# Kernel optimization log

Measured on AMD Instinct MI355X. Metric: run time of the kernel, lower is better.

## Reference

```python
import jax, jax.numpy as jnp
from jax import lax
import numpy as np

B, C, H, W = 16, 128, 128, 128
S1 = C // 2   # 64, LKA3 branch channels
S2 = C - S1   # 64, LKA5 branch channels
EPS = 1e-6
DN = ('NCHW', 'OIHW', 'NCHW')


def _dw(x, w, b, pad, dil=1):
    # depthwise conv; torch weight layout (C,1,kh,kw) == OIHW with groups=C
    y = lax.conv_general_dilated(x, w, (1, 1), [(pad[0], pad[0]), (pad[1], pad[1])],
                                 rhs_dilation=(dil, dil), dimension_numbers=DN,
                                 feature_group_count=w.shape[0])
    return y + b[None, :, None, None]


def _pw(x, w, b):
    # 1x1 pointwise conv
    y = lax.conv_general_dilated(x, w, (1, 1), [(0, 0), (0, 0)], dimension_numbers=DN)
    return y + b[None, :, None, None]


def setup_inputs() -> dict:
    key = jax.random.key(0)
    ks = iter(jax.random.split(key, 40))
    rn = lambda shape, s=0.05: jax.random.normal(next(ks), shape, jnp.float32) * s
    inp = {
        'x': jax.random.normal(next(ks), (B, C, H, W), jnp.float32),
        'ln_w': jnp.ones((C,), jnp.float32),
        'ln_b': jnp.zeros((C,), jnp.float32),
        'scale': rn((1, C, 1, 1)),
        'pf_w': rn((2 * C, C, 1, 1)), 'pf_b': rn((2 * C,)),
        # LKA3: dw(1x3) -> dw(3x1) -> dw5 dil2 -> 1x1
        'lka3_w1': rn((S1, 1, 1, 3)), 'lka3_b1': rn((S1,)),
        'lka3_w2': rn((S1, 1, 3, 1)), 'lka3_b2': rn((S1,)),
        'lka3_w3': rn((S1, 1, 5, 5)), 'lka3_b3': rn((S1,)),
        'lka3_w4': rn((S1, S1, 1, 1)), 'lka3_b4': rn((S1,)),
        # LKA5: dw5 -> dw7 dil2 -> 1x1
        'lka5_w1': rn((S2, 1, 5, 5)), 'lka5_b1': rn((S2,)),
        'lka5_w2': rn((S2, 1, 7, 7)), 'lka5_b2': rn((S2,)),
        'lka5_w3': rn((S2, S2, 1, 1)), 'lka5_b3': rn((S2,)),
        # gating convs
        'x3a_w': rn((S1, 1, 1, 3)), 'x3a_b': rn((S1,)),
        'x3b_w': rn((S1, 1, 3, 1)), 'x3b_b': rn((S1,)),
        'x5_w': rn((S2, 1, 5, 5)), 'x5_b': rn((S2,)),
        'pl_w': rn((C, C, 1, 1)), 'pl_b': rn((C,)),
    }
    return inp


def reference(x, ln_w, ln_b, scale, pf_w, pf_b,
              lka3_w1, lka3_b1, lka3_w2, lka3_b2, lka3_w3, lka3_b3, lka3_w4, lka3_b4,
              lka5_w1, lka5_b1, lka5_w2, lka5_b2, lka5_w3, lka5_b3,
              x3a_w, x3a_b, x3b_w, x3b_b, x5_w, x5_b, pl_w, pl_b):
    shortcut = x
    # channels_first LayerNorm (biased variance over channel dim)
    u = jnp.mean(x, axis=1, keepdims=True)
    s = jnp.mean((x - u) ** 2, axis=1, keepdims=True)
    xn = (x - u) * lax.rsqrt(s + EPS)
    xn = ln_w[None, :, None, None] * xn + ln_b[None, :, None, None]
    # proj_first: C -> 2C
    h = _pw(xn, pf_w, pf_b)
    a, xh = h[:, :C], h[:, C:]
    a1, a2 = a[:, :S1], a[:, S1:]
    # gating branch for a1: 1x3 then 3x1 depthwise
    x3_out = _dw(_dw(a1, x3a_w, x3a_b, (0, 1)), x3b_w, x3b_b, (1, 0))
    # LKA3: dw(1x3)->dw(3x1)->dw5(dil2,pad4)->1x1
    l3 = _dw(a1, lka3_w1, lka3_b1, (0, 1))
    l3 = _dw(l3, lka3_w2, lka3_b2, (1, 0))
    l3 = _dw(l3, lka3_w3, lka3_b3, (4, 4), dil=2)
    l3 = _pw(l3, lka3_w4, lka3_b4)
    attn_1 = l3 * x3_out
    # LKA5: dw5(pad2)->dw7(dil2,pad6)->1x1
    l5 = _dw(a2, lka5_w1, lka5_b1, (2, 2))
    l5 = _dw(l5, lka5_w2, lka5_b2, (6, 6), dil=2)
    l5 = _pw(l5, lka5_w3, lka5_b3)
    attn_2 = l5 * _dw(a2, x5_w, x5_b, (2, 2))
    a = jnp.concatenate([attn_1, attn_2], axis=1)
    out = _pw(xh * a, pl_w, pl_b) * scale + shortcut
    return out
```

## Files before the change

kernel.cpp:

```cpp
#include <hip/hip_runtime.h>
#include <hip/hip_bf16.h>

typedef __hip_bfloat16 bf16;
typedef unsigned short ushort_t;
typedef float f32x4 __attribute__((ext_vector_type(4)));
typedef short bf16x8 __attribute__((ext_vector_type(8)));

#define MFMA16(a, b, c) __builtin_amdgcn_mfma_f32_16x16x32_bf16(a, b, c, 0, 0, 0)

__device__ inline ushort_t f2b(float f) {
  bf16 h = __float2bfloat16(f);
  return __builtin_bit_cast(ushort_t, h);
}
__device__ inline float b2f(ushort_t u) {
  bf16 h = __builtin_bit_cast(bf16, u);
  return __bfloat162float(h);
}
__device__ inline float blo(unsigned d) { return __builtin_bit_cast(float, d << 16); }
__device__ inline float bhi(unsigned d) { return __builtin_bit_cast(float, d & 0xffff0000u); }


__global__ __launch_bounds__(256) void prepack_pf(
    const float* __restrict__ pf_w, ushort_t* __restrict__ pf_wp)
{
  int idx = blockIdx.x * 256 + threadIdx.x;
  int j = idx & 7, lane = (idx >> 3) & 63, kc = (idx >> 9) & 3, t = idx >> 11;
  int oc = t * 16 + (lane & 15), ic = kc * 32 + (lane >> 4) * 8 + j;
  pf_wp[idx] = f2b(pf_w[oc * 128 + ic]);
}

__global__ __launch_bounds__(256) void prepack_small(
    const float* __restrict__ w4, const float* __restrict__ w5,
    const float* __restrict__ plw, ushort_t* __restrict__ dst)
{
  int idx = blockIdx.x * 256 + threadIdx.x;
  if (idx < 8192) {
    const float* src = (idx < 4096) ? w4 : w5;
    int k = idx & 4095;
    int j = k & 7, lane = (k >> 3) & 63, kc = (k >> 9) & 1, t = k >> 10;
    int oc = t * 16 + (lane & 15), ic = kc * 32 + (lane >> 4) * 8 + j;
    dst[idx] = f2b(src[oc * 64 + ic]);
  } else {
    int k = idx - 8192;
    int j = k & 7, lane = (k >> 3) & 63, kc = (k >> 9) & 3, t = k >> 11;
    int oc = t * 16 + (lane & 15), ic = kc * 32 + (lane >> 4) * 8 + j;
    dst[idx] = f2b(plw[oc * 128 + ic]);
  }
}

__global__ __launch_bounds__(256) void ln_pf_mfma(
    const float* __restrict__ x, const float* __restrict__ ln_w,
    const float* __restrict__ ln_b, const ushort_t* __restrict__ pf_wp,
    const float* __restrict__ pf_b, ushort_t* __restrict__ h)
{
  __shared__ __attribute__((aligned(16))) unsigned char sm[34816];
  ushort_t* xs = (ushort_t*)sm;
  float* red = (float*)(sm + 17408);
  float* mrs = (float*)(sm + 17408 + 2048);

  const int tid = threadIdx.x;
  const int p = tid & 63, cg = tid >> 6;
  const int g0 = blockIdx.x * 64;
  const int b = g0 >> 14, hw0 = g0 & 16383;
  const float* xp = x + (long)b * (128L * 16384) + hw0 + p;

  float v[32];
  #pragma unroll
  for (int i = 0; i < 32; ++i) v[i] = xp[(long)(cg * 32 + i) * 16384];
  float s = 0.f, ss = 0.f;
  #pragma unroll
  for (int i = 0; i < 32; ++i) { s += v[i]; ss += v[i] * v[i]; }
  red[cg * 64 + p] = s;
  red[256 + cg * 64 + p] = ss;
  __syncthreads();
  if (tid < 64) {
    float st = red[tid] + red[64 + tid] + red[128 + tid] + red[192 + tid];
    float sst = red[256 + tid] + red[320 + tid] + red[384 + tid] + red[448 + tid];
    float m = st * 0.0078125f;
    float var = sst * 0.0078125f - m * m;
    mrs[tid] = m;
    mrs[64 + tid] = rsqrtf(var + 1e-6f);
  }
  __syncthreads();
  {
    float m = mrs[p], rs = mrs[64 + p];
    #pragma unroll
    for (int i = 0; i < 32; ++i) {
      int c = cg * 32 + i;
      xs[p * 136 + c] = f2b((v[i] - m) * rs * ln_w[c] + ln_b[c]);
    }
  }
  __syncthreads();

  const int l = tid & 63, lm = l & 15, q = l >> 4;
  const int wv = __builtin_amdgcn_readfirstlane(tid >> 6);
  f32x4 acc[4][4];
  #pragma unroll
  for (int a = 0; a < 4; ++a)
    #pragma unroll
    for (int n = 0; n < 4; ++n) acc[a][n] = {0.f, 0.f, 0.f, 0.f};

  #pragma unroll
  for (int kc = 0; kc < 4; ++kc) {
    bf16x8 af[4], bfr[4];
    #pragma unroll
    for (int mt = 0; mt < 4; ++mt)
      af[mt] = *(const bf16x8*)&xs[(mt * 16 + lm) * 136 + kc * 32 + q * 8];
    #pragma unroll
    for (int nt = 0; nt < 4; ++nt)
      bfr[nt] = *(const bf16x8*)&pf_wp[(((wv * 4 + nt) * 4 + kc) * 64 + l) * 8];
    #pragma unroll
    for (int mt = 0; mt < 4; ++mt)
      #pragma unroll
      for (int nt = 0; nt < 4; ++nt)
        acc[mt][nt] = MFMA16(af[mt], bfr[nt], acc[mt][nt]);
  }
  __syncthreads();

  ushort_t* hst = (ushort_t*)sm;
  #pragma unroll
  for (int nt = 0; nt < 4; ++nt) {
    int oc = wv * 64 + nt * 16 + lm;
    float bias = pf_b[oc];
    #pragma unroll
    for (int mt = 0; mt < 4; ++mt) {
      int px0 = mt * 16 + q * 4;
      union { ushort_t u[4]; uint2 w; } pk;
      #pragma unroll
      for (int r = 0; r < 4; ++r) pk.u[r] = f2b(acc[mt][nt][r] + bias);
      *(uint2*)&hst[oc * 68 + px0] = pk.w;
    }
  }
  __syncthreads();
  {
    int px = (tid & 31) * 2;
    int ocb = tid >> 5;
    ushort_t* hp = h + (long)b * 256 * 16384 + hw0 + px;
    #pragma unroll
    for (int i = 0; i < 32; ++i) {
      int oc = ocb + 8 * i;
      *(unsigned*)(hp + (long)oc * 16384) = *(unsigned*)&hst[oc * 68 + px];
    }
  }
}

__global__ __launch_bounds__(256) void dw_branch1_kernel(
    const bf16* __restrict__ hbuf,
    const float* __restrict__ w1, const float* __restrict__ b1,
    const float* __restrict__ w2, const float* __restrict__ b2,
    const float* __restrict__ w3, const float* __restrict__ b3,
    const float* __restrict__ wa, const float* __restrict__ ba,
    const float* __restrict__ wb, const float* __restrict__ bb,
    bf16* __restrict__ d3, bf16* __restrict__ x3o)
{
  __shared__ float sa[18 * 138];
  __shared__ float st1[18 * 136];
  __shared__ float st2[16 * 136];
  __shared__ float su1[10 * 128];

  const int t = blockIdx.x;
  const int band = t & 15, c = (t >> 4) & 63, b = t >> 10;
  const int y0 = band * 8;
  const int tid = threadIdx.x;
  const int col = tid & 127, rhalf = tid >> 7;
  const bf16* ap = hbuf + ((long)b * 256 + c) * 16384;

  float W1[3], W2[3], WA[3], WB[3], W3[25];
  #pragma unroll
  for (int k = 0; k < 3; ++k) {
    W1[k] = w1[c * 3 + k]; W2[k] = w2[c * 3 + k];
    WA[k] = wa[c * 3 + k]; WB[k] = wb[c * 3 + k];
  }
  #pragma unroll
  for (int k = 0; k < 25; ++k) W3[k] = w3[c * 25 + k];
  const float B1 = b1[c], B2 = b2[c], B3 = b3[c], BA = ba[c], BB = bb[c];

  for (int i = tid; i < 18 * 5; i += 256) {
    int r = i / 5, qq = i % 5;
    sa[r * 138 + qq] = 0.f;
    sa[r * 138 + 133 + qq] = 0.f;
  }
  #pragma unroll
  for (int rr = rhalf; rr < 18; rr += 2) {
    int gy = y0 - 5 + rr;
    float v = 0.f;
    if ((unsigned)gy < 128u) v = __bfloat162float(ap[gy * 128 + col]);
    sa[rr * 138 + 5 + col] = v;
  }
  __syncthreads();

  #pragma unroll
  for (int rr = rhalf; rr < 18; rr += 2) {
    int gy = y0 - 5 + rr;
    bool rowok = (unsigned)gy < 128u;
    const float* sr = &sa[rr * 138];
    {
      int xq = col - 4;
      float v = W1[0] * sr[col] + W1[1] * sr[col + 1] + W1[2] * sr[col + 2] + B1;
      st1[rr * 136 + col] = (rowok && (unsigned)xq < 128u) ? v : 0.f;
    }
    if (col < 8) {
      int cc = col + 128, xq = cc - 4;
      float v = W1[0] * sr[cc] + W1[1] * sr[cc + 1] + W1[2] * sr[cc + 2] + B1;
      st1[rr * 136 + cc] = (rowok && (unsigned)xq < 128u) ? v : 0.f;
    }
  }
  #pragma unroll
  for (int r = rhalf; r < 10; r += 2) {
    int gy = y0 - 1 + r;
    const float* sr = &sa[(r + 4) * 138];
    float v = WA[0] * sr[col + 4] + WA[1] * sr[col + 5] + WA[2] * sr[col + 6] + BA;
    su1[r * 128 + col] = ((unsigned)gy < 128u) ? v : 0.f;
  }
  __syncthreads();

  #pragma unroll
  for (int r = rhalf; r < 16; r += 2) {
    int gy = y0 - 4 + r;
    bool rowok = (unsigned)gy < 128u;
    {
      int xq = col - 4;
      float v = W2[0] * st1[r * 136 + col] + W2[1] * st1[(r + 1) * 136 + col] +
                W2[2] * st1[(r + 2) * 136 + col] + B2;
      st2[r * 136 + col] = (rowok && (unsigned)xq < 128u) ? v : 0.f;
    }
    if (col < 8) {
      int cc = col + 128, xq = cc - 4;
      float v = W2[0] * st1[r * 136 + cc] + W2[1] * st1[(r + 1) * 136 + cc] +
                W2[2] * st1[(r + 2) * 136 + cc] + B2;
      st2[r * 136 + cc] = (rowok && (unsigned)xq < 128u) ? v : 0.f;
    }
  }
  __syncthreads();

  bf16* d3p = d3 + ((long)b * 64 + c) * 16384;
  bf16* x3p = x3o + ((long)b * 64 + c) * 16384;
  #pragma unroll
  for (int ro = rhalf; ro < 8; ro += 2) {
    float acc = B3;
    #pragma unroll
    for (int u = 0; u < 5; ++u)
      #pragma unroll
      for (int v = 0; v < 5; ++v)
        acc += W3[u * 5 + v] * st2[(ro + 2 * u) * 136 + col + 2 * v];
    d3p[(y0 + ro) * 128 + col] = __float2bfloat16(acc);

    float xo = WB[0] * su1[ro * 128 + col] + WB[1] * su1[(ro + 1) * 128 + col] +
               WB[2] * su1[(ro + 2) * 128 + col] + BB;
    x3p[(y0 + ro) * 128 + col] = __float2bfloat16(xo);
  }
}

__global__ __launch_bounds__(256) void dw_branch2_kernel(
    const bf16* __restrict__ hbuf,
    const float* __restrict__ w1, const float* __restrict__ b1,
    const float* __restrict__ w2, const float* __restrict__ b2,
    const float* __restrict__ w5, const float* __restrict__ b5,
    bf16* __restrict__ d5, bf16* __restrict__ x5o)
{
  __shared__ ushort_t sa[32 * 160];
  __shared__ float sv[28 * 148];

  const int t = blockIdx.x;
  const int band = t & 7, c = (t >> 3) & 63, b = t >> 9;
  const int y0 = band * 16;
  const int tid = threadIdx.x;
  const bf16* ap = hbuf + ((long)b * 256 + 64 + c) * 16384;

  unsigned* sad = (unsigned*)sa;
  for (int i = tid; i < 32 * 16; i += 256) {
    int r = i >> 4, j = i & 15;
    int dw = (j < 4) ? j : (64 + j);
    sad[r * 80 + dw] = 0u;
  }
  {
    const int lane = tid & 63, w = tid >> 6;
    #pragma unroll
    for (int i = 0; i < 8; ++i) {
      int rr = w + 4 * i;
      int gy = y0 - 8 + rr;
      unsigned val = 0u;
      if ((unsigned)gy < 128u) val = *(const unsigned*)(ap + gy * 128 + lane * 2);
      sad[rr * 80 + 4 + lane] = val;
    }
  }
  __syncthreads();

  {
    float W[25];
    #pragma unroll
    for (int k = 0; k < 25; ++k) W[k] = w1[c * 25 + k];
    const float B1v = b1[c];
    for (int task = tid; task < 28 * 18; task += 256) {
      int r = task / 18, g = task - r * 18;
      int c0 = g * 8;
      float acc[8];
      #pragma unroll
      for (int j = 0; j < 8; ++j) acc[j] = B1v;
      #pragma unroll
      for (int u = 0; u < 5; ++u) {
        const unsigned* sr = sad + (r + u) * 80 + (c0 >> 1);
        unsigned e0 = sr[0], e1 = sr[1], e2 = sr[2], e3 = sr[3], e4 = sr[4], e5 = sr[5];
        float vw[12];
        vw[0] = blo(e0); vw[1] = bhi(e0); vw[2] = blo(e1); vw[3] = bhi(e1);
        vw[4] = blo(e2); vw[5] = bhi(e2); vw[6] = blo(e3); vw[7] = bhi(e3);
        vw[8] = blo(e4); vw[9] = bhi(e4); vw[10] = blo(e5); vw[11] = bhi(e5);
        #pragma unroll
        for (int v5 = 0; v5 < 5; ++v5)
          #pragma unroll
          for (int j = 0; j < 8; ++j)
            acc[j] += W[u * 5 + v5] * vw[j + v5];
      }
      int gy = y0 - 6 + r;
      bool rok = (unsigned)gy < 128u;
      float* svr = &sv[r * 148 + c0];
      #pragma unroll
      for (int j = 0; j < 8; ++j) {
        int xx = c0 + j - 6;
        svr[j] = (rok && (unsigned)xx < 128u) ? acc[j] : 0.f;
      }
    }
  }

  const int tx = tid & 15, ty = tid >> 4;
  const int x0 = tx * 8;
  const int y = y0 + ty;

  {
    float W[25];
    #pragma unroll
    for (int k = 0; k < 25; ++k) W[k] = w5[c * 25 + k];
    float acc[8];
    #pragma unroll
    for (int j = 0; j < 8; ++j) acc[j] = b5[c];
    #pragma unroll
    for (int u = 0; u < 5; ++u) {
      const unsigned* sr = sad + (ty + 6 + u) * 80 + (x0 >> 1);
      unsigned e0 = sr[3], e1 = sr[4], e2 = sr[5], e3 = sr[6], e4 = sr[7], e5 = sr[8];
      float vw[12];
      vw[0] = blo(e0); vw[1] = bhi(e0); vw[2] = blo(e1); vw[3] = bhi(e1);
      vw[4] = blo(e2); vw[5] = bhi(e2); vw[6] = blo(e3); vw[7] = bhi(e3);
      vw[8] = blo(e4); vw[9] = bhi(e4); vw[10] = blo(e5); vw[11] = bhi(e5);
      #pragma unroll
      for (int v5 = 0; v5 < 5; ++v5)
        #pragma unroll
        for (int j = 0; j < 8; ++j)
          acc[j] += W[u * 5 + v5] * vw[j + v5];
    }
    union { ushort_t u[8]; uint4 v; } pk;
    #pragma unroll
    for (int j = 0; j < 8; ++j) pk.u[j] = f2b(acc[j]);
    bf16* x5p = x5o + ((long)b * 64 + c) * 16384;
    *(uint4*)(x5p + y * 128 + x0) = pk.v;
  }
  __syncthreads();

  {
    float W[49];
    #pragma unroll
    for (int k = 0; k < 49; ++k) W[k] = w2[c * 49 + k];
    float acc[8];
    #pragma unroll
    for (int j = 0; j < 8; ++j) acc[j] = b2[c];
    #pragma unroll
    for (int u = 0; u < 7; ++u) {
      const float* svr = &sv[(ty + 2 * u) * 148 + x0];
      float vw[20];
      #pragma unroll
      for (int k = 0; k < 20; ++k) vw[k] = svr[k];
      #pragma unroll
      for (int vv = 0; vv < 7; ++vv)
        #pragma unroll
        for (int j = 0; j < 8; ++j)
          acc[j] += W[u * 7 + vv] * vw[j + 2 * vv];
    }
    union { ushort_t u[8]; uint4 v; } pk;
    #pragma unroll
    for (int j = 0; j < 8; ++j) pk.u[j] = f2b(acc[j]);
    bf16* d5p = d5 + ((long)b * 64 + c) * 16384;
    *(uint4*)(d5p + y * 128 + x0) = pk.v;
  }
}

__global__ __launch_bounds__(256) void final_mfma(
    const ushort_t* __restrict__ h, const ushort_t* __restrict__ d3,
    const ushort_t* __restrict__ x3o, const ushort_t* __restrict__ d5,
    const ushort_t* __restrict__ x5o,
    const ushort_t* __restrict__ w4p, const float* __restrict__ b4,
    const ushort_t* __restrict__ w5p, const float* __restrict__ b5,
    const ushort_t* __restrict__ plwp, const float* __restrict__ plb,
    const float* __restrict__ scale, const float* __restrict__ x,
    float* __restrict__ out)
{
  __shared__ __attribute__((aligned(16))) unsigned char sm[35840];
  ushort_t* A3 = (ushort_t*)sm;
  ushort_t* A5 = (ushort_t*)(sm + 9216);
  ushort_t* gA = (ushort_t*)(sm + 18432);

  const int tid = threadIdx.x;
  const int g0 = blockIdx.x * 64;
  const int b = g0 >> 14, hw0 = g0 & 16383;
  const long base64 = (long)b * 64 * 16384 + hw0;
  const long base256 = (long)b * 256 * 16384 + hw0;
  const int p = tid & 63;

  #pragma unroll
  for (int i = 0; i < 16; ++i) {
    int ch = (tid >> 6) + 4 * i;
    A3[p * 72 + ch] = d3[base64 + (long)ch * 16384 + p];
    A5[p * 72 + ch] = d5[base64 + (long)ch * 16384 + p];
  }
  __syncthreads();

  const int l = tid & 63, lm = l & 15, q = l >> 4;
  const int wv = __builtin_amdgcn_readfirstlane(tid >> 6);

  f32x4 ac1[4], ac2[4];
  #pragma unroll
  for (int n = 0; n < 4; ++n) { ac1[n] = {0.f,0.f,0.f,0.f}; ac2[n] = {0.f,0.f,0.f,0.f}; }
  #pragma unroll
  for (int kc = 0; kc < 2; ++kc) {
    bf16x8 a3f = *(const bf16x8*)&A3[(wv * 16 + lm) * 72 + kc * 32 + q * 8];
    bf16x8 a5f = *(const bf16x8*)&A5[(wv * 16 + lm) * 72 + kc * 32 + q * 8];
    #pragma unroll
    for (int nt = 0; nt < 4; ++nt) {
      bf16x8 bw4 = *(const bf16x8*)&w4p[((nt * 2 + kc) * 64 + l) * 8];
      bf16x8 bw5 = *(const bf16x8*)&w5p[((nt * 2 + kc) * 64 + l) * 8];
      ac1[nt] = MFMA16(a3f, bw4, ac1[nt]);
      ac2[nt] = MFMA16(a5f, bw5, ac2[nt]);
    }
  }

  #pragma unroll
  for (int nt = 0; nt < 4; ++nt) {
    int oc = nt * 16 + lm;
    float bb1 = b4[oc], bb2 = b5[oc];
    #pragma unroll
    for (int r = 0; r < 4; ++r) {
      int px = wv * 16 + q * 4 + r;
      float at1 = (ac1[nt][r] + bb1) * b2f(x3o[base64 + (long)oc * 16384 + px]);
      float at2 = (ac2[nt][r] + bb2) * b2f(x5o[base64 + (long)oc * 16384 + px]);
      float g1 = b2f(h[base256 + (long)(128 + oc) * 16384 + px]) * at1;
      float g2 = b2f(h[base256 + (long)(192 + oc) * 16384 + px]) * at2;
      gA[px * 136 + oc]      = f2b(g1);
      gA[px * 136 + 64 + oc] = f2b(g2);
    }
  }
  __syncthreads();

  f32x4 ap[4][2];
  #pragma unroll
  for (int mt = 0; mt < 4; ++mt) { ap[mt][0] = {0.f,0.f,0.f,0.f}; ap[mt][1] = {0.f,0.f,0.f,0.f}; }
  #pragma unroll
  for (int kc = 0; kc < 4; ++kc) {
    bf16x8 af[4];
    #pragma unroll
    for (int mt = 0; mt < 4; ++mt)
      af[mt] = *(const bf16x8*)&gA[(mt * 16 + lm) * 136 + kc * 32 + q * 8];
    #pragma unroll
    for (int j = 0; j < 2; ++j) {
      bf16x8 bp = *(const bf16x8*)&plwp[(((wv * 2 + j) * 4 + kc) * 64 + l) * 8];
      #pragma unroll
      for (int mt = 0; mt < 4; ++mt)
        ap[mt][j] = MFMA16(af[mt], bp, ap[mt][j]);
    }
  }
  __syncthreads();

  float* outL = (float*)sm;
  #pragma unroll
  for (int j = 0; j < 2; ++j) {
    int oc = (wv * 2 + j) * 16 + lm;
    float sc = scale[oc], bb = plb[oc];
    #pragma unroll
    for (int mt = 0; mt < 4; ++mt) {
      int px0 = mt * 16 + q * 4;
      f32x4 vv;
      #pragma unroll
      for (int r = 0; r < 4; ++r) vv[r] = (ap[mt][j][r] + bb) * sc;
      *(f32x4*)&outL[oc * 68 + px0] = vv;
    }
  }
  __syncthreads();
  {
    const float* xp = x + (long)b * 128 * 16384 + hw0 + p;
    float* op = out + (long)b * 128 * 16384 + hw0 + p;
    #pragma unroll
    for (int i = 0; i < 32; ++i) {
      int oc = (tid >> 6) + 4 * i;
      op[(long)oc * 16384] = outL[oc * 68 + p] + xp[(long)oc * 16384];
    }
  }
}

extern "C" void kernel_launch(void* const* d_in, const int* in_sizes, int n_in,
                              void* d_out, int out_size, void* d_ws, size_t ws_size,
                              hipStream_t stream)
{
  (void)in_sizes; (void)n_in; (void)out_size; (void)ws_size;
  const float* x       = (const float*)d_in[0];
  const float* ln_w    = (const float*)d_in[1];
  const float* ln_b    = (const float*)d_in[2];
  const float* scale   = (const float*)d_in[3];
  const float* pf_w    = (const float*)d_in[4];
  const float* pf_b    = (const float*)d_in[5];
  const float* lka3_w1 = (const float*)d_in[6];
  const float* lka3_b1 = (const float*)d_in[7];
  const float* lka3_w2 = (const float*)d_in[8];
  const float* lka3_b2 = (const float*)d_in[9];
  const float* lka3_w3 = (const float*)d_in[10];
  const float* lka3_b3 = (const float*)d_in[11];
  const float* lka3_w4 = (const float*)d_in[12];
  const float* lka3_b4 = (const float*)d_in[13];
  const float* lka5_w1 = (const float*)d_in[14];
  const float* lka5_b1 = (const float*)d_in[15];
  const float* lka5_w2 = (const float*)d_in[16];
  const float* lka5_b2 = (const float*)d_in[17];
  const float* lka5_w3 = (const float*)d_in[18];
  const float* lka5_b3 = (const float*)d_in[19];
  const float* x3a_w   = (const float*)d_in[20];
  const float* x3a_b   = (const float*)d_in[21];
  const float* x3b_w   = (const float*)d_in[22];
  const float* x3b_b   = (const float*)d_in[23];
  const float* x5_w    = (const float*)d_in[24];
  const float* x5_b    = (const float*)d_in[25];
  const float* pl_w    = (const float*)d_in[26];
  const float* pl_b    = (const float*)d_in[27];
  float* out = (float*)d_out;

  bf16* h   = (bf16*)d_ws;
  bf16* d3  = h + 67108864L;
  bf16* x3o = d3 + 16777216L;
  bf16* d5  = x3o + 16777216L;
  bf16* x5o = d5 + 16777216L;
  ushort_t* pf_wp = (ushort_t*)d_out;
  ushort_t* wsmall = (ushort_t*)d_ws;

  dim3 blk(256);

  prepack_pf<<<128, blk, 0, stream>>>(pf_w, pf_wp);
  ln_pf_mfma<<<4096, blk, 0, stream>>>(x, ln_w, ln_b, pf_wp, pf_b, (ushort_t*)h);

  dw_branch1_kernel<<<16384, blk, 0, stream>>>(
      h, lka3_w1, lka3_b1, lka3_w2, lka3_b2, lka3_w3, lka3_b3,
      x3a_w, x3a_b, x3b_w, x3b_b, d3, x3o);

  dw_branch2_kernel<<<8192, blk, 0, stream>>>(
      h, lka5_w1, lka5_b1, lka5_w2, lka5_b2, x5_w, x5_b, d5, x5o);

  prepack_small<<<96, blk, 0, stream>>>(lka3_w4, lka5_w3, pl_w, wsmall);

  final_mfma<<<4096, blk, 0, stream>>>(
      (const ushort_t*)h, (const ushort_t*)d3, (const ushort_t*)x3o,
      (const ushort_t*)d5, (const ushort_t*)x5o,
      wsmall, lka3_b4, wsmall + 4096, lka5_b3,
      wsmall + 8192, pl_b, scale, x, out);
}
```

Baseline: 589.7 us.

## Restructure LKA3 depthwise branch kernel with 16-row bands and 8-pixel register tiles

Rewrites the first depthwise branch kernel so each block handles a 16-row band instead of 8. This halves the grid and cuts redundant halo reloads. The input tile is kept as packed bf16 in shared memory, and each thread computes 8 horizontal outputs from registers with 16-byte vector stores. Shared memory is aliased between stages to fit, and the gating path now reads straight from the input tile. In exchange, register use and the shared footprint per block go up, which may lower occupancy.

New measurement: 537.0 us. -8.9%, faster.

```diff
diff --git a/kernel.cpp b/kernel.cpp
--- a/kernel.cpp
+++ b/kernel.cpp
@@ -153,101 +153,143 @@
     const float* __restrict__ wb, const float* __restrict__ bb,
     bf16* __restrict__ d3, bf16* __restrict__ x3o)
 {
-  __shared__ float sa[18 * 138];
-  __shared__ float st1[18 * 136];
-  __shared__ float st2[16 * 136];
-  __shared__ float su1[10 * 128];
+  __shared__ __attribute__((aligned(16))) unsigned char smem[28000];
+  float* st1 = (float*)smem;
+  float* st2 = (float*)(smem + 14560);
+  ushort_t* sa = (ushort_t*)(smem + 14560);
+  unsigned* sad = (unsigned*)sa;
 
   const int t = blockIdx.x;
-  const int band = t & 15, c = (t >> 4) & 63, b = t >> 10;
-  const int y0 = band * 8;
+  const int band = t & 7, c = (t >> 3) & 63, b = t >> 9;
+  const int y0 = band * 16;
   const int tid = threadIdx.x;
-  const int col = tid & 127, rhalf = tid >> 7;
   const bf16* ap = hbuf + ((long)b * 256 + c) * 16384;
 
-  float W1[3], W2[3], WA[3], WB[3], W3[25];
-  #pragma unroll
-  for (int k = 0; k < 3; ++k) {
-    W1[k] = w1[c * 3 + k]; W2[k] = w2[c * 3 + k];
-    WA[k] = wa[c * 3 + k]; WB[k] = wb[c * 3 + k];
-  }
-  #pragma unroll
-  for (int k = 0; k < 25; ++k) W3[k] = w3[c * 25 + k];
-  const float B1 = b1[c], B2 = b2[c], B3 = b3[c], BA = ba[c], BB = bb[c];
-
-  for (int i = tid; i < 18 * 5; i += 256) {
-    int r = i / 5, qq = i % 5;
-    sa[r * 138 + qq] = 0.f;
-    sa[r * 138 + 133 + qq] = 0.f;
-  }
-  #pragma unroll
-  for (int rr = rhalf; rr < 18; rr += 2) {
-    int gy = y0 - 5 + rr;
-    float v = 0.f;
-    if ((unsigned)gy < 128u) v = __bfloat162float(ap[gy * 128 + col]);
-    sa[rr * 138 + 5 + col] = v;
-  }
-  __syncthreads();
-
-  #pragma unroll
-  for (int rr = rhalf; rr < 18; rr += 2) {
-    int gy = y0 - 5 + rr;
-    bool rowok = (unsigned)gy < 128u;
-    const float* sr = &sa[rr * 138];
-    {
-      int xq = col - 4;
-      float v = W1[0] * sr[col] + W1[1] * sr[col + 1] + W1[2] * sr[col + 2] + B1;
-      st1[rr * 136 + col] = (rowok && (unsigned)xq < 128u) ? v : 0.f;
-    }
-    if (col < 8) {
-      int cc = col + 128, xq = cc - 4;
-      float v = W1[0] * sr[cc] + W1[1] * sr[cc + 1] + W1[2] * sr[cc + 2] + B1;
-      st1[rr * 136 + cc] = (rowok && (unsigned)xq < 128u) ? v : 0.f;
-    }
-  }
-  #pragma unroll
-  for (int r = rhalf; r < 10; r += 2) {
-    int gy = y0 - 1 + r;
-    const float* sr = &sa[(r + 4) * 138];
-    float v = WA[0] * sr[col + 4] + WA[1] * sr[col + 5] + WA[2] * sr[col + 6] + BA;
-    su1[r * 128 + col] = ((unsigned)gy < 128u) ? v : 0.f;
-  }
-  __syncthreads();
-
-  #pragma unroll
-  for (int r = rhalf; r < 16; r += 2) {
-    int gy = y0 - 4 + r;
-    bool rowok = (unsigned)gy < 128u;
-    {
-      int xq = col - 4;
-      float v = W2[0] * st1[r * 136 + col] + W2[1] * st1[(r + 1) * 136 + col] +
-                W2[2] * st1[(r + 2) * 136 + col] + B2;
-      st2[r * 136 + col] = (rowok && (unsigned)xq < 128u) ? v : 0.f;
-    }
-    if (col < 8) {
-      int cc = col + 128, xq = cc - 4;
-      float v = W2[0] * st1[r * 136 + cc] + W2[1] * st1[(r + 1) * 136 + cc] +
-                W2[2] * st1[(r + 2) * 136 + cc] + B2;
-      st2[r * 136 + cc] = (rowok && (unsigned)xq < 128u) ? v : 0.f;
-    }
-  }
-  __syncthreads();
-
-  bf16* d3p = d3 + ((long)b * 64 + c) * 16384;
-  bf16* x3p = x3o + ((long)b * 64 + c) * 16384;
-  #pragma unroll
-  for (int ro = rhalf; ro < 8; ro += 2) {
-    float acc = B3;
-    #pragma unroll
-    for (int u = 0; u < 5; ++u)
-      #pragma unroll
-      for (int v = 0; v < 5; ++v)
-        acc += W3[u * 5 + v] * st2[(ro + 2 * u) * 136 + col + 2 * v];
-    d3p[(y0 + ro) * 128 + col] = __float2bfloat16(acc);
-
-    float xo = WB[0] * su1[ro * 128 + col] + WB[1] * su1[(ro + 1) * 128 + col] +
-               WB[2] * su1[(ro + 2) * 128 + col] + BB;
-    x3p[(y0 + ro) * 128 + col] = __float2bfloat16(xo);
+  for (int i = tid; i < 26 * 16; i += 256) {
+    int r = i >> 4, j = i & 15;
+    int dw = (j < 4) ? j : (64 + j);
+    sad[r * 80 + dw] = 0u;
+  }
+  {
+    const int lane = tid & 63, w = tid >> 6;
+    #pragma unroll
+    for (int i = 0; i < 7; ++i) {
+      int rr = w + 4 * i;
+      if (rr < 26) {
+        int gy = y0 - 5 + rr;
+        unsigned val = 0u;
+        if ((unsigned)gy < 128u) val = *(const unsigned*)(ap + gy * 128 + lane * 2);
+        sad[rr * 80 + 4 + lane] = val;
+      }
+    }
+  }
+  __syncthreads();
+
+  {
+    float W0 = w1[c * 3], Wm = w1[c * 3 + 1], Wp = w1[c * 3 + 2];
+    const float B1v = b1[c];
+    for (int task = tid; task < 26 * 17; task += 256) {
+      int r = task / 17, g = task - r * 17;
+      int c0 = g * 8;
+      const unsigned* sr = sad + r * 80 + (c0 >> 1) + 1;
+      unsigned e0 = sr[0], e1 = sr[1], e2 = sr[2], e3 = sr[3], e4 = sr[4], e5 = sr[5];
+      float vw[12];
+      vw[0] = blo(e0); vw[1] = bhi(e0); vw[2] = blo(e1); vw[3] = bhi(e1);
+      vw[4] = blo(e2); vw[5] = bhi(e2); vw[6] = blo(e3); vw[7] = bhi(e3);
+      vw[8] = blo(e4); vw[9] = bhi(e4); vw[10] = blo(e5); vw[11] = bhi(e5);
+      int gy = y0 - 5 + r;
+      bool rok = (unsigned)gy < 128u;
+      float* dst = &st1[r * 140 + c0];
+      #pragma unroll
+      for (int j = 0; j < 8; ++j) {
+        float v = W0 * vw[j + 1] + Wm * vw[j + 2] + Wp * vw[j + 3] + B1v;
+        int xx = c0 - 4 + j;
+        dst[j] = (rok && (unsigned)xx < 128u) ? v : 0.f;
+      }
+    }
+  }
+
+  const int tx = tid & 15, ty = tid >> 4;
+  const int x0 = tx * 8;
+  const int y = y0 + ty;
+
+  {
+    float A0 = wa[c * 3], A1 = wa[c * 3 + 1], A2 = wa[c * 3 + 2];
+    float Bv0 = wb[c * 3], Bv1 = wb[c * 3 + 1], Bv2 = wb[c * 3 + 2];
+    const float BAv = ba[c], BBv = bb[c];
+    float su[3][8];
+    #pragma unroll
+    for (int dy = 0; dy < 3; ++dy) {
+      int gy2 = y - 1 + dy;
+      int srow = ty + 4 + dy;
+      const unsigned* sr = sad + srow * 80 + (x0 >> 1) + 3;
+      unsigned e0 = sr[0], e1 = sr[1], e2 = sr[2], e3 = sr[3], e4 = sr[4], e5 = sr[5];
+      float vw[12];
+      vw[0] = blo(e0); vw[1] = bhi(e0); vw[2] = blo(e1); vw[3] = bhi(e1);
+      vw[4] = blo(e2); vw[5] = bhi(e2); vw[6] = blo(e3); vw[7] = bhi(e3);
+      vw[8] = blo(e4); vw[9] = bhi(e4); vw[10] = blo(e5); vw[11] = bhi(e5);
+      bool rok = (unsigned)gy2 < 128u;
+      #pragma unroll
+      for (int j = 0; j < 8; ++j) {
+        float v = A0 * vw[j + 1] + A1 * vw[j + 2] + A2 * vw[j + 3] + BAv;
+        su[dy][j] = rok ? v : 0.f;
+      }
+    }
+    union { ushort_t u[8]; uint4 v; } pk;
+    #pragma unroll
+    for (int j = 0; j < 8; ++j)
+      pk.u[j] = f2b(Bv0 * su[0][j] + Bv1 * su[1][j] + Bv2 * su[2][j] + BBv);
+    bf16* x3p = x3o + ((long)b * 64 + c) * 16384;
+    *(uint4*)(x3p + y * 128 + x0) = pk.v;
+  }
+  __syncthreads();
+
+  {
+    float W0 = w2[c * 3], Wm = w2[c * 3 + 1], Wp = w2[c * 3 + 2];
+    const float B2v = b2[c];
+    for (int task = tid; task < 24 * 17; task += 256) {
+      int q = task / 17, g = task - q * 17;
+      int c0 = g * 8;
+      const float* r0 = &st1[q * 140 + c0];
+      const float* r1 = &st1[(q + 1) * 140 + c0];
+      const float* r2 = &st1[(q + 2) * 140 + c0];
+      int gy = y0 - 4 + q;
+      bool rok = (unsigned)gy < 128u;
+      float* dst = &st2[q * 140 + c0];
+      #pragma unroll
+      for (int j = 0; j < 8; ++j) {
+        float v = W0 * r0[j] + Wm * r1[j] + Wp * r2[j] + B2v;
+        int xx = c0 - 4 + j;
+        dst[j] = (rok && (unsigned)xx < 128u) ? v : 0.f;
+      }
+    }
+  }
+  __syncthreads();
+
+  {
+    float W[25];
+    #pragma unroll
+    for (int k = 0; k < 25; ++k) W[k] = w3[c * 25 + k];
+    float acc[8];
+    #pragma unroll
+    for (int j = 0; j < 8; ++j) acc[j] = b3[c];
+    #pragma unroll
+    for (int u = 0; u < 5; ++u) {
+      const float* svr = &st2[(ty + 2 * u) * 140 + x0];
+      float vw[16];
+      #pragma unroll
+      for (int k = 0; k < 16; ++k) vw[k] = svr[k];
+      #pragma unroll
+      for (int vv = 0; vv < 5; ++vv)
+        #pragma unroll
+        for (int j = 0; j < 8; ++j)
+          acc[j] += W[u * 5 + vv] * vw[j + 2 * vv];
+    }
+    union { ushort_t u[8]; uint4 v; } pk;
+    #pragma unroll
+    for (int j = 0; j < 8; ++j) pk.u[j] = f2b(acc[j]);
+    bf16* d3p = d3 + ((long)b * 64 + c) * 16384;
+    *(uint4*)(d3p + y * 128 + x0) = pk.v;
   }
 }
 
@@ -541,7 +583,7 @@
   prepack_pf<<<128, blk, 0, stream>>>(pf_w, pf_wp);
   ln_pf_mfma<<<4096, blk, 0, stream>>>(x, ln_w, ln_b, pf_wp, pf_b, (ushort_t*)h);
 
-  dw_branch1_kernel<<<16384, blk, 0, stream>>>(
+  dw_branch1_kernel<<<8192, blk, 0, stream>>>(
       h, lka3_w1, lka3_b1, lka3_w2, lka3_b2, lka3_w3, lka3_b3,
       x3a_w, x3a_b, x3b_w, x3b_b, d3, x3o);
 
```
